# Kernel optimization log

Measured on AMD Instinct MI355X. Metric: run time of the kernel, lower is better.

The kernel has to match this reference:

```python
import jax, jax.numpy as jnp
import numpy as np

E, CAP, D = 32, 4096, 256
H = 4 * D  # hidden_dim = 4*d_model


def setup_inputs() -> dict:
    key = jax.random.key(0)
    k1, k2, k3 = jax.random.split(key, 3)
    x = jax.random.normal(k1, (E, CAP, D), dtype=jnp.float32)
    w_fc = jax.random.normal(k2, (E, D, H), dtype=jnp.float32) * (1.0 / np.sqrt(D))
    w_proj = jax.random.normal(k3, (E, H, D), dtype=jnp.float32) * (1.0 / np.sqrt(H))
    return {"x": x, "w_fc": w_fc, "w_proj": w_proj}


def reference(x, w_fc, w_proj):
    # h = bmm(x, w_fc): [E, cap, d] @ [E, d, 4d] -> [E, cap, 4d]
    h = jnp.einsum('ecd,edh->ech', x, w_fc)
    # exact GELU (torch nn.GELU default uses erf form)
    h = jax.nn.gelu(h, approximate=False)
    # out = bmm(h, w_proj): [E, cap, 4d] @ [E, 4d, d] -> [E, cap, d]
    out = jnp.einsum('ech,ehd->ecd', h, w_proj)
    # dropout is identity in eval mode (p=0.0 here)
    return out
```

## Files before the change

kernel.cpp:

```cpp
#include <hip/hip_runtime.h>
#include <cstdint>
#include <cstddef>


#define NE   32
#define CAPN 4096
#define DDIM 256
#define HDIM 1024

typedef __bf16 bf16x8 __attribute__((ext_vector_type(8)));
typedef __bf16 bf16x4 __attribute__((ext_vector_type(4)));
typedef __bf16 bf16x2 __attribute__((ext_vector_type(2)));
typedef float  f32x4  __attribute__((ext_vector_type(4)));

#define B_XS   0
#define B_HC   65536
#define B_STG  98304
#define LDS160 163840

#define AS1 __attribute__((address_space(1)))
#define AS3 __attribute__((address_space(3)))

__device__ __forceinline__ void gld_lds16(const void* g, void* l) {
  __builtin_amdgcn_global_load_lds((const AS1 uint32_t*)g, (AS3 uint32_t*)l, 16, 0, 0);
}

__device__ __forceinline__ float gelu_f(float x) {
  float x2 = x * x;
  float u  = x * __builtin_fmaf(0.1029432f, x2, 2.3022078f);
  float t  = __builtin_amdgcn_exp2f(u);
  float r  = __builtin_amdgcn_rcpf(t + 1.0f);
  return __builtin_fmaf(-x, r, x);
}

#define WAITV(n) asm volatile("s_waitcnt vmcnt(" #n ") lgkmcnt(0)" ::: "memory")
#define LGKM0()  asm volatile("s_waitcnt lgkmcnt(0)" ::: "memory")
#define BAR()    do { __builtin_amdgcn_s_barrier(); __builtin_amdgcn_sched_barrier(0); } while (0)

__global__ __launch_bounds__(256) void tcast_kernel(const float* __restrict__ in,
                                                    __bf16* __restrict__ outp,
                                                    int R, int C) {
  __shared__ __bf16 tl[64][72];
  const int cb = C >> 6;
  const int nb = (R >> 6) * cb;
  const int b  = blockIdx.x;
  const int e  = b / nb;
  const int t  = b - e * nb;
  const int br = t / cb;
  const int bc = t - br * cb;
  const float* src = in + ((size_t)e * R + (size_t)br * 64) * C + (size_t)bc * 64;
#pragma unroll
  for (int i = 0; i < 16; ++i) {
    int idx = i * 256 + threadIdx.x;
    int r = idx >> 6, c = idx & 63;
    tl[c][r] = (__bf16)src[(size_t)r * C + c];
  }
  __syncthreads();
  __bf16* dst = outp + ((size_t)e * C + (size_t)bc * 64) * R + (size_t)br * 64;
#pragma unroll
  for (int i = 0; i < 8; ++i) {
    int idx = i * 512 + threadIdx.x * 2;
    int c = idx >> 6, r = idx & 63;
    bf16x2 p;
    p[0] = tl[c][r];
    p[1] = tl[c][r + 1];
    *(bf16x2*)(dst + (size_t)c * R + r) = p;
  }
}

__global__ __launch_bounds__(512, 1) void fused_mlp(
    const float* __restrict__ x, const __bf16* __restrict__ wfcT,
    const __bf16* __restrict__ wprojT, float* __restrict__ out) {
  extern __shared__ char smem[];
  const int tid  = threadIdx.x;
  const int lane = tid & 63;
  const int l15  = lane & 15;
  const int l4   = lane >> 4;
  const int l7   = l15 & 7;
  const int w    = tid >> 6;
  const int wm   = w & 1;
  const int q    = w >> 1;
  const int e    = blockIdx.x >> 5;
  const int m0   = (blockIdx.x & 31) << 7;

  const int physA  = l4 ^ ((l15 >> 1) & 3);
  const int aOff0  = (q * 32 + l15) * 64 + physA * 16;
  const int mRow   = wm * 64 + l15;
  const int bxOff0 = mRow * 64 + physA * 16;
  const int hcOff0 = mRow * 256;
  const int pl     = l4 ^ l7;

  const float* xbase = x + ((size_t)(e * CAPN + m0)) * DDIM;
  const int xm    = tid >> 2;
  const int xsl   = tid & 3;
  const int xphys = xsl ^ ((xm >> 1) & 3);

  auto stage_slab = [&](int s) {
    const int buf = s & 3;
    const int c   = s >> 4;
    const int t   = s & 15;
    const __bf16* base;
    size_t rs;
    if (t < 8) {
      base = wfcT + ((size_t)(e * HDIM + c * 256)) * DDIM + t * 32;
      rs   = DDIM;
    } else {
      base = wprojT + ((size_t)(e * DDIM)) * HDIM + c * 256 + ((t >> 2) & 1) * 128 + (t & 3) * 32;
      rs   = HDIM;
    }
#pragma unroll
    for (int i = 0; i < 2; ++i) {
      int o  = tid + i * 512;
      int r  = o >> 2;
      int sl = (o & 3) ^ ((r >> 1) & 3);
      gld_lds16(base + (size_t)r * rs + sl * 8, &smem[B_STG + buf * 16384 + o * 16]);
    }
  };

  float4 xb0_[8], xb1_[8];

#define XLOAD(P) do {                                                          \
    const float* xs_ = xbase + (size_t)xm * DDIM + (P) * 32 + xsl * 8;         \
    xb0_[P] = *(const float4*)xs_;                                             \
    xb1_[P] = *(const float4*)(xs_ + 4);                                       \
  } while (0)

#define XCONV(P) do {                                                          \
    bf16x8 v_;                                                                 \
    v_[0] = (__bf16)xb0_[P].x; v_[1] = (__bf16)xb0_[P].y;                      \
    v_[2] = (__bf16)xb0_[P].z; v_[3] = (__bf16)xb0_[P].w;                      \
    v_[4] = (__bf16)xb1_[P].x; v_[5] = (__bf16)xb1_[P].y;                      \
    v_[6] = (__bf16)xb1_[P].z; v_[7] = (__bf16)xb1_[P].w;                      \
    *(bf16x8*)(&smem[B_XS + (P) * 8192 + xm * 64 + xphys * 16]) = v_;          \
  } while (0)

  f32x4 zero = 0.0f;
  f32x4 acc1[4][4], acc2[4][4];
#pragma unroll
  for (int a = 0; a < 4; ++a)
#pragma unroll
    for (int b = 0; b < 4; ++b) acc2[a][b] = zero;

#define ZERO_ACC1() do {                                                       \
    _Pragma("unroll") for (int a_ = 0; a_ < 4; ++a_)                           \
      _Pragma("unroll") for (int b_ = 0; b_ < 4; ++b_) acc1[a_][b_] = zero;    \
  } while (0)

#define P1SLAB(BUF, DS) do {                                                   \
    bf16x8 af_[4], bx_[4];                                                     \
    const char* sb_ = &smem[B_STG + (BUF) * 16384];                            \
    _Pragma("unroll") for (int f_ = 0; f_ < 4; ++f_)                           \
      af_[f_] = *(const bf16x8*)(sb_ + aOff0 + (f_ & 1) * 1024 + (f_ >> 1) * 8192); \
    const char* xs_ = &smem[B_XS + (DS) * 8192 + bxOff0];                      \
    _Pragma("unroll") for (int fm_ = 0; fm_ < 4; ++fm_)                        \
      bx_[fm_] = *(const bf16x8*)(xs_ + fm_ * 1024);                           \
    __builtin_amdgcn_s_setprio(1);                                             \
    _Pragma("unroll") for (int f_ = 0; f_ < 4; ++f_)                           \
      _Pragma("unroll") for (int fm_ = 0; fm_ < 4; ++fm_)                      \
        acc1[f_][fm_] = __builtin_amdgcn_mfma_f32_16x16x32_bf16(af_[f_], bx_[fm_], acc1[f_][fm_], 0, 0, 0); \
    __builtin_amdgcn_s_setprio(0);                                             \
  } while (0)

#define P2SLAB(BUF, HS) do {                                                   \
    bf16x8 af_[4], bx_[4];                                                     \
    const char* sb_ = &smem[B_STG + (BUF) * 16384];                            \
    _Pragma("unroll") for (int f_ = 0; f_ < 4; ++f_)                           \
      af_[f_] = *(const bf16x8*)(sb_ + aOff0 + (f_ & 1) * 1024 + (f_ >> 1) * 8192); \
    const int p_ = ((((HS) & 2) ? 8 : 0)) | (pl ^ (((HS) & 1) * 4));           \
    _Pragma("unroll") for (int fm_ = 0; fm_ < 4; ++fm_)                        \
      bx_[fm_] = *(const bf16x8*)(&smem[B_HC + hcOff0 + fm_ * 4096 + p_ * 16]); \
    __builtin_amdgcn_s_setprio(1);                                             \
    _Pragma("unroll") for (int f_ = 0; f_ < 4; ++f_)                           \
      _Pragma("unroll") for (int fm_ = 0; fm_ < 4; ++fm_)                      \
        acc2[f_][fm_] = __builtin_amdgcn_mfma_f32_16x16x32_bf16(af_[f_], bx_[fm_], acc2[f_][fm_], 0, 0, 0); \
    __builtin_amdgcn_s_setprio(0);                                             \
  } while (0)

#define GELU_HALF(G) do {                                                      \
    _Pragma("unroll") for (int f2_ = 0; f2_ < 2; ++f2_) {                      \
      const int s_ = q * 4 + f2_ * 2 + (l4 >> 1);                              \
      const int p_ = (s_ & 8) | ((s_ & 7) ^ l7);                               \
      _Pragma("unroll") for (int fm_ = 0; fm_ < 4; ++fm_) {                    \
        bf16x4 hv_;                                                            \
        _Pragma("unroll") for (int j_ = 0; j_ < 4; ++j_)                       \
          hv_[j_] = (__bf16)gelu_f(acc1[(G) * 2 + f2_][fm_][j_]);              \
        *(bf16x4*)(&smem[B_HC + hcOff0 + fm_ * 4096 + p_ * 16 + (l4 & 1) * 8]) = hv_; \
      }                                                                        \
    }                                                                          \
  } while (0)

#define W_C0(T, VM) do {                                                       \
    WAITV(VM); BAR();                                                          \
    stage_slab((T) + 3);                                                       \
    if ((T) <= 4) XLOAD((T) + 3);                                              \
    P1SLAB((T) & 3, (T));                                                      \
    if ((T) <= 6) XCONV((T) + 1);                                              \
  } while (0)

#define W_P1(C, T) do {                                                        \
    WAITV(4); BAR();                                                           \
    stage_slab((C) * 16 + (T) + 3);                                            \
    P1SLAB((T) & 3, (T));                                                      \
  } while (0)

#define W_P2(C, T, VM) do {                                                    \
    WAITV(VM); BAR();                                                          \
    if ((C) * 16 + (T) + 3 < 64) stage_slab((C) * 16 + (T) + 3);               \
    P2SLAB((T) & 3, ((T) - 8) & 3);                                            \
  } while (0)

#define W_P2G(C) do {   \
    WAITV(4); BAR();                                                           \
    stage_slab((C) * 16 + 15);                                                 \
    GELU_HALF(1);                                                              \
    LGKM0(); BAR();                                                            \
    P2SLAB(0, 0);                                                              \
  } while (0)

#define CHUNK_TAIL(C, VM14, VM15) do {                                         \
    GELU_HALF(0);                                                              \
    W_P2((C), 8, 4); W_P2((C), 9, 4); W_P2((C), 10, 4); W_P2((C), 11, 4);      \
    W_P2G(C);                                                                  \
    W_P2((C), 13, 4); W_P2((C), 14, VM14); W_P2((C), 15, VM15);                \
  } while (0)

  XLOAD(0); XLOAD(1); XLOAD(2);
  stage_slab(0); stage_slab(1); stage_slab(2);
  XCONV(0);

  ZERO_ACC1();
  W_C0(0, 4); W_C0(1, 6); W_C0(2, 8); W_C0(3, 10);
  W_C0(4, 10); W_C0(5, 10); W_C0(6, 8); W_C0(7, 6);
  CHUNK_TAIL(0, 4, 4);

  for (int c = 1; c < 3; ++c) {
    ZERO_ACC1();
    W_P1(c, 0); W_P1(c, 1); W_P1(c, 2); W_P1(c, 3);
    W_P1(c, 4); W_P1(c, 5); W_P1(c, 6); W_P1(c, 7);
    CHUNK_TAIL(c, 4, 4);
  }

  ZERO_ACC1();
  W_P1(3, 0); W_P1(3, 1); W_P1(3, 2); W_P1(3, 3);
  W_P1(3, 4); W_P1(3, 5); W_P1(3, 6); W_P1(3, 7);
  CHUNK_TAIL(3, 2, 0);

#pragma unroll
  for (int f = 0; f < 4; ++f) {
#pragma unroll
    for (int fm = 0; fm < 4; ++fm) {
      int m = m0 + mRow + fm * 16;
      int d = q * 32 + (f & 1) * 16 + (f >> 1) * 128 + l4 * 4;
      *(f32x4*)(out + ((size_t)(e * CAPN + m)) * DDIM + d) = acc2[f][fm];
    }
  }
}

extern "C" void kernel_launch(void* const* d_in, const int* in_sizes, int n_in,
                              void* d_out, int out_size, void* d_ws, size_t ws_size,
                              hipStream_t stream) {
  (void)in_sizes; (void)n_in; (void)out_size; (void)ws_size;
  const float* x     = (const float*)d_in[0];
  const float* wfc   = (const float*)d_in[1];
  const float* wproj = (const float*)d_in[2];
  float* out = (float*)d_out;

  __bf16* wfcT   = (__bf16*)d_ws;
  __bf16* wprojT = (__bf16*)((char*)d_ws + (size_t)NE * DDIM * HDIM * sizeof(__bf16));

  hipFuncSetAttribute((const void*)fused_mlp,
                      hipFuncAttributeMaxDynamicSharedMemorySize, LDS160);

  tcast_kernel<<<dim3(NE * 64), dim3(256), 0, stream>>>(wfc, wfcT, DDIM, HDIM);
  tcast_kernel<<<dim3(NE * 64), dim3(256), 0, stream>>>(wproj, wprojT, HDIM, DDIM);
  fused_mlp<<<dim3(NE * 32), dim3(512), LDS160, stream>>>(x, wfcT, wprojT, out);
}
```

Baseline: 221.2 us.

## Software-pipeline LDS fragment loads with double-buffered register sets across MFMA slabs

Splits each slab step into separate fragment-load and MFMA phases, using two register sets (A/B) so the LDS reads for the next slab are issued right after the current slab's MFMAs and overlap them. The staging schedule is deepened (one more slab in flight, waits changed to vmcnt(2)) and the x-conversion in the first chunk is advanced by one step. This aims to hide LDS read latency behind matrix-core work. In exchange it raises register pressure with a second fragment set and makes the barrier and buffer-reuse ordering more delicate, so reads could race with staging writes.

```diff
diff --git a/kernel.cpp b/kernel.cpp
--- a/kernel.cpp
+++ b/kernel.cpp
@@ -36,6 +36,7 @@
 #define WAITV(n) asm volatile("s_waitcnt vmcnt(" #n ") lgkmcnt(0)" ::: "memory")
 #define LGKM0()  asm volatile("s_waitcnt lgkmcnt(0)" ::: "memory")
 #define BAR()    do { __builtin_amdgcn_s_barrier(); __builtin_amdgcn_sched_barrier(0); } while (0)
+#define SB0()    __builtin_amdgcn_sched_barrier(0)
 
 __global__ __launch_bounds__(256) void tcast_kernel(const float* __restrict__ in,
                                                     __bf16* __restrict__ outp,
@@ -146,33 +147,31 @@
       _Pragma("unroll") for (int b_ = 0; b_ < 4; ++b_) acc1[a_][b_] = zero;    \
   } while (0)
 
-#define P1SLAB(BUF, DS) do {                                                   \
-    bf16x8 af_[4], bx_[4];                                                     \
-    const char* sb_ = &smem[B_STG + (BUF) * 16384];                            \
+  bf16x8 afA[4], bxA[4], afB[4], bxB[4];
+
+#define PRE_AF(SET, BUF_) do {                                                 \
+    const char* sb_ = &smem[B_STG + (BUF_) * 16384];                           \
     _Pragma("unroll") for (int f_ = 0; f_ < 4; ++f_)                           \
-      af_[f_] = *(const bf16x8*)(sb_ + aOff0 + (f_ & 1) * 1024 + (f_ >> 1) * 8192); \
-    const char* xs_ = &smem[B_XS + (DS) * 8192 + bxOff0];                      \
+      af##SET[f_] = *(const bf16x8*)(sb_ + aOff0 + (f_ & 1) * 1024 + (f_ >> 1) * 8192); \
+  } while (0)
+
+#define PRE_BX1(SET, DS_) do {                                                 \
+    const char* xs_ = &smem[B_XS + (DS_) * 8192 + bxOff0];                     \
     _Pragma("unroll") for (int fm_ = 0; fm_ < 4; ++fm_)                        \
-      bx_[fm_] = *(const bf16x8*)(xs_ + fm_ * 1024);                           \
+      bx##SET[fm_] = *(const bf16x8*)(xs_ + fm_ * 1024);                       \
+  } while (0)
+
+#define PRE_BX2(SET, HS_) do {                                                 \
+    const int p_ = (((HS_) & 2) ? 8 : 0) | (pl ^ (((HS_) & 1) * 4));           \
+    _Pragma("unroll") for (int fm_ = 0; fm_ < 4; ++fm_)                        \
+      bx##SET[fm_] = *(const bf16x8*)(&smem[B_HC + hcOff0 + fm_ * 4096 + p_ * 16]); \
+  } while (0)
+
+#define MFMA16(SET, ACC) do {                                                  \
     __builtin_amdgcn_s_setprio(1);                                             \
     _Pragma("unroll") for (int f_ = 0; f_ < 4; ++f_)                           \
       _Pragma("unroll") for (int fm_ = 0; fm_ < 4; ++fm_)                      \
-        acc1[f_][fm_] = __builtin_amdgcn_mfma_f32_16x16x32_bf16(af_[f_], bx_[fm_], acc1[f_][fm_], 0, 0, 0); \
-    __builtin_amdgcn_s_setprio(0);                                             \
-  } while (0)
-
-#define P2SLAB(BUF, HS) do {                                                   \
-    bf16x8 af_[4], bx_[4];                                                     \
-    const char* sb_ = &smem[B_STG + (BUF) * 16384];                            \
-    _Pragma("unroll") for (int f_ = 0; f_ < 4; ++f_)                           \
-      af_[f_] = *(const bf16x8*)(sb_ + aOff0 + (f_ & 1) * 1024 + (f_ >> 1) * 8192); \
-    const int p_ = ((((HS) & 2) ? 8 : 0)) | (pl ^ (((HS) & 1) * 4));           \
-    _Pragma("unroll") for (int fm_ = 0; fm_ < 4; ++fm_)                        \
-      bx_[fm_] = *(const bf16x8*)(&smem[B_HC + hcOff0 + fm_ * 4096 + p_ * 16]); \
-    __builtin_amdgcn_s_setprio(1);                                             \
-    _Pragma("unroll") for (int f_ = 0; f_ < 4; ++f_)                           \
-      _Pragma("unroll") for (int fm_ = 0; fm_ < 4; ++fm_)                      \
-        acc2[f_][fm_] = __builtin_amdgcn_mfma_f32_16x16x32_bf16(af_[f_], bx_[fm_], acc2[f_][fm_], 0, 0, 0); \
+        ACC[f_][fm_] = __builtin_amdgcn_mfma_f32_16x16x32_bf16(af##SET[f_], bx##SET[fm_], ACC[f_][fm_], 0, 0, 0); \
     __builtin_amdgcn_s_setprio(0);                                             \
   } while (0)
 
@@ -189,61 +188,73 @@
     }                                                                          \
   } while (0)
 
-#define W_C0(T, VM) do {                                                       \
-    WAITV(VM); BAR();                                                          \
-    stage_slab((T) + 3);                                                       \
-    if ((T) <= 4) XLOAD((T) + 3);                                              \
-    P1SLAB((T) & 3, (T));                                                      \
-    if ((T) <= 6) XCONV((T) + 1);                                              \
-  } while (0)
-
-#define W_P1(C, T) do {                                                        \
-    WAITV(4); BAR();                                                           \
-    stage_slab((C) * 16 + (T) + 3);                                            \
-    P1SLAB((T) & 3, (T));                                                      \
-  } while (0)
-
-#define W_P2(C, T, VM) do {                                                    \
-    WAITV(VM); BAR();                                                          \
-    if ((C) * 16 + (T) + 3 < 64) stage_slab((C) * 16 + (T) + 3);               \
-    P2SLAB((T) & 3, ((T) - 8) & 3);                                            \
-  } while (0)
-
-#define W_P2G(C) do {   \
-    WAITV(4); BAR();                                                           \
-    stage_slab((C) * 16 + 15);                                                 \
-    GELU_HALF(1);                                                              \
-    LGKM0(); BAR();                                                            \
-    P2SLAB(0, 0);                                                              \
-  } while (0)
-
-#define CHUNK_TAIL(C, VM14, VM15) do {                                         \
-    GELU_HALF(0);                                                              \
-    W_P2((C), 8, 4); W_P2((C), 9, 4); W_P2((C), 10, 4); W_P2((C), 11, 4);      \
-    W_P2G(C);                                                                  \
-    W_P2((C), 13, 4); W_P2((C), 14, VM14); W_P2((C), 15, VM15);                \
-  } while (0)
-
+#define CHUNK_HEAD(C_) do {                                                    \
+    WAITV(2); BAR(); MFMA16(A, acc1); stage_slab((C_)*16 + 3);  PRE_AF(B, 1); PRE_BX1(B, 1); \
+    WAITV(2); BAR(); MFMA16(B, acc1); stage_slab((C_)*16 + 4);  PRE_AF(A, 2); PRE_BX1(A, 2); \
+    WAITV(2); BAR(); MFMA16(A, acc1); stage_slab((C_)*16 + 5);  PRE_AF(B, 3); PRE_BX1(B, 3); \
+    WAITV(2); BAR(); MFMA16(B, acc1); stage_slab((C_)*16 + 6);  PRE_AF(A, 0); PRE_BX1(A, 4); \
+    WAITV(2); BAR(); MFMA16(A, acc1); stage_slab((C_)*16 + 7);  PRE_AF(B, 1); PRE_BX1(B, 5); \
+    WAITV(2); BAR(); MFMA16(B, acc1); stage_slab((C_)*16 + 8);  PRE_AF(A, 2); PRE_BX1(A, 6); \
+    WAITV(2); BAR(); MFMA16(A, acc1); stage_slab((C_)*16 + 9);  PRE_AF(B, 3); PRE_BX1(B, 7); \
+  } while (0)
+
+#define CHUNK_TAIL7(C_, LAST_) do {                                            \
+    WAITV(2); BAR(); MFMA16(B, acc1); GELU_HALF(0);                            \
+      stage_slab((C_)*16 + 10); PRE_AF(A, 0);                                  \
+    WAITV(2); BAR(); PRE_BX2(A, 0); MFMA16(A, acc2);                           \
+      stage_slab((C_)*16 + 11); PRE_AF(B, 1); PRE_BX2(B, 1);                   \
+    WAITV(2); BAR(); MFMA16(B, acc2); stage_slab((C_)*16 + 12);                \
+      PRE_AF(A, 2); PRE_BX2(A, 2);                                             \
+    WAITV(2); BAR(); MFMA16(A, acc2); stage_slab((C_)*16 + 13);                \
+      PRE_AF(B, 3); PRE_BX2(B, 3);                                             \
+    WAITV(2); BAR(); MFMA16(B, acc2); stage_slab((C_)*16 + 14);                \
+      PRE_AF(A, 0);                                                            \
+    WAITV(2); BAR(); GELU_HALF(1); ZERO_ACC1(); LGKM0(); BAR();                \
+      PRE_BX2(A, 0); MFMA16(A, acc2); stage_slab((C_)*16 + 15);                \
+      PRE_AF(B, 1); PRE_BX2(B, 1);                                             \
+    WAITV(2); BAR(); MFMA16(B, acc2);                                          \
+      if (!(LAST_)) stage_slab((C_)*16 + 16);                                  \
+      PRE_AF(A, 2); PRE_BX2(A, 2);                                             \
+    if (LAST_) { WAITV(0); } else { WAITV(2); }                                \
+    BAR(); MFMA16(A, acc2);                                                    \
+      if (!(LAST_)) stage_slab((C_)*16 + 17);                                  \
+      PRE_AF(B, 3); PRE_BX2(B, 3);                                             \
+    if (LAST_) { WAITV(0); } else { WAITV(2); }                                \
+    BAR(); MFMA16(B, acc2);                                                    \
+      if (!(LAST_)) { stage_slab((C_)*16 + 18); PRE_AF(A, 0); PRE_BX1(A, 0); } \
+  } while (0)
+
+  ZERO_ACC1();
   XLOAD(0); XLOAD(1); XLOAD(2);
+  SB0();
   stage_slab(0); stage_slab(1); stage_slab(2);
-  XCONV(0);
-
-  ZERO_ACC1();
-  W_C0(0, 4); W_C0(1, 6); W_C0(2, 8); W_C0(3, 10);
-  W_C0(4, 10); W_C0(5, 10); W_C0(6, 8); W_C0(7, 6);
-  CHUNK_TAIL(0, 4, 4);
+  XCONV(0); XCONV(1);
+
+  WAITV(2); BAR();
+  PRE_AF(A, 0); PRE_BX1(A, 0);
+  MFMA16(A, acc1);
+  stage_slab(3); SB0(); XLOAD(3); PRE_AF(B, 1); PRE_BX1(B, 1); XCONV(2);
+  WAITV(4); BAR(); MFMA16(B, acc1);
+  stage_slab(4); SB0(); XLOAD(4); PRE_AF(A, 2); PRE_BX1(A, 2); XCONV(3);
+  WAITV(6); BAR(); MFMA16(A, acc1);
+  stage_slab(5); SB0(); XLOAD(5); PRE_AF(B, 3); PRE_BX1(B, 3); XCONV(4);
+  WAITV(6); BAR(); MFMA16(B, acc1);
+  stage_slab(6); SB0(); XLOAD(6); PRE_AF(A, 0); PRE_BX1(A, 4); XCONV(5);
+  WAITV(6); BAR(); MFMA16(A, acc1);
+  stage_slab(7); SB0(); XLOAD(7); PRE_AF(B, 1); PRE_BX1(B, 5); XCONV(6);
+  WAITV(6); BAR(); MFMA16(B, acc1);
+  stage_slab(8); PRE_AF(A, 2); PRE_BX1(A, 6); XCONV(7);
+  WAITV(4); BAR(); MFMA16(A, acc1);
+  stage_slab(9); PRE_AF(B, 3); PRE_BX1(B, 7);
+  CHUNK_TAIL7(0, 0);
 
   for (int c = 1; c < 3; ++c) {
-    ZERO_ACC1();
-    W_P1(c, 0); W_P1(c, 1); W_P1(c, 2); W_P1(c, 3);
-    W_P1(c, 4); W_P1(c, 5); W_P1(c, 6); W_P1(c, 7);
-    CHUNK_TAIL(c, 4, 4);
-  }
-
-  ZERO_ACC1();
-  W_P1(3, 0); W_P1(3, 1); W_P1(3, 2); W_P1(3, 3);
-  W_P1(3, 4); W_P1(3, 5); W_P1(3, 6); W_P1(3, 7);
-  CHUNK_TAIL(3, 2, 0);
+    CHUNK_HEAD(c);
+    CHUNK_TAIL7(c, 0);
+  }
+
+  CHUNK_HEAD(3);
+  CHUNK_TAIL7(3, 1);
 
 #pragma unroll
   for (int f = 0; f < 4; ++f) {
```

After: 216.5 us. 1.02x faster.

## Software-pipeline LDS fragment reads with double-buffered registers across MFMA steps

Applied to the files above, without the earlier changes.

Restructures the fused MoE MLP main loop so the LDS fragment loads for the next slab go into a second register set while the current slab's MFMAs run. The stage-slab lambda is replaced by precomputed per-thread global offsets in specialized FC and projection staging macros. Most waits drop the lgkmcnt(0) requirement, leaving only vmcnt waits. This is meant to hide LDS latency and cut address arithmetic, at the cost of more VGPRs for the double fragment registers and tighter correctness dependencies between buffer reuse and barriers.

```diff
diff --git a/kernel.cpp b/kernel.cpp
--- a/kernel.cpp
+++ b/kernel.cpp
@@ -33,9 +33,12 @@
   return __builtin_fmaf(-x, r, x);
 }
 
-#define WAITV(n) asm volatile("s_waitcnt vmcnt(" #n ") lgkmcnt(0)" ::: "memory")
-#define LGKM0()  asm volatile("s_waitcnt lgkmcnt(0)" ::: "memory")
-#define BAR()    do { __builtin_amdgcn_s_barrier(); __builtin_amdgcn_sched_barrier(0); } while (0)
+#define WV_(n)  asm volatile("s_waitcnt vmcnt(" #n ")" ::: "memory")
+#define WV(n)   WV_(n)
+#define WVL_(n) asm volatile("s_waitcnt vmcnt(" #n ") lgkmcnt(0)" ::: "memory")
+#define WVL(n)  WVL_(n)
+#define LGKM0() asm volatile("s_waitcnt lgkmcnt(0)" ::: "memory")
+#define BAR()   do { __builtin_amdgcn_s_barrier(); __builtin_amdgcn_sched_barrier(0); } while (0)
 
 __global__ __launch_bounds__(256) void tcast_kernel(const float* __restrict__ in,
                                                     __bf16* __restrict__ outp,
@@ -90,32 +93,31 @@
   const int hcOff0 = mRow * 256;
   const int pl     = l4 ^ l7;
 
+  const int rr  = tid >> 2;
+  const int ssl = (tid & 3) ^ ((rr >> 1) & 3);
+  const int gofsFC = rr * DDIM + ssl * 8;
+  const int gofsPJ = rr * HDIM + ssl * 8;
+  const __bf16* wfcT_e   = wfcT   + (size_t)e * HDIM * DDIM;
+  const __bf16* wprojT_e = wprojT + (size_t)e * DDIM * HDIM;
+  char* ldsStg0 = smem + B_STG + tid * 16;
+
   const float* xbase = x + ((size_t)(e * CAPN + m0)) * DDIM;
   const int xm    = tid >> 2;
   const int xsl   = tid & 3;
   const int xphys = xsl ^ ((xm >> 1) & 3);
 
-  auto stage_slab = [&](int s) {
-    const int buf = s & 3;
-    const int c   = s >> 4;
-    const int t   = s & 15;
-    const __bf16* base;
-    size_t rs;
-    if (t < 8) {
-      base = wfcT + ((size_t)(e * HDIM + c * 256)) * DDIM + t * 32;
-      rs   = DDIM;
-    } else {
-      base = wprojT + ((size_t)(e * DDIM)) * HDIM + c * 256 + ((t >> 2) & 1) * 128 + (t & 3) * 32;
-      rs   = HDIM;
-    }
-#pragma unroll
-    for (int i = 0; i < 2; ++i) {
-      int o  = tid + i * 512;
-      int r  = o >> 2;
-      int sl = (o & 3) ^ ((r >> 1) & 3);
-      gld_lds16(base + (size_t)r * rs + sl * 8, &smem[B_STG + buf * 16384 + o * 16]);
-    }
-  };
+#define STAGE_FC(C_, T_) do {                                                  \
+    const __bf16* s0_ = wfcT_e + (size_t)(C_) * (256 * DDIM) + (T_) * 32 + gofsFC; \
+    gld_lds16(s0_,              ldsStg0 + ((T_) & 3) * 16384);                 \
+    gld_lds16(s0_ + 128 * DDIM, ldsStg0 + ((T_) & 3) * 16384 + 8192);          \
+  } while (0)
+
+#define STAGE_PJ(C_, T_) do {                                                  \
+    const __bf16* s0_ = wprojT_e + (size_t)(C_) * 256 +                        \
+                        (((T_) >> 2) & 1) * 128 + ((T_) & 3) * 32 + gofsPJ;    \
+    gld_lds16(s0_,              ldsStg0 + ((T_) & 3) * 16384);                 \
+    gld_lds16(s0_ + 128 * HDIM, ldsStg0 + ((T_) & 3) * 16384 + 8192);          \
+  } while (0)
 
   float4 xb0_[8], xb1_[8];
 
@@ -139,40 +141,38 @@
 #pragma unroll
   for (int a = 0; a < 4; ++a)
 #pragma unroll
-    for (int b = 0; b < 4; ++b) acc2[a][b] = zero;
+    for (int b = 0; b < 4; ++b) { acc1[a][b] = zero; acc2[a][b] = zero; }
 
 #define ZERO_ACC1() do {                                                       \
     _Pragma("unroll") for (int a_ = 0; a_ < 4; ++a_)                           \
       _Pragma("unroll") for (int b_ = 0; b_ < 4; ++b_) acc1[a_][b_] = zero;    \
   } while (0)
 
-#define P1SLAB(BUF, DS) do {                                                   \
-    bf16x8 af_[4], bx_[4];                                                     \
-    const char* sb_ = &smem[B_STG + (BUF) * 16384];                            \
+  bf16x8 afR0[4], bxR0[4], afR1[4], bxR1[4];
+
+#define PAF(S_, BUF_) do {                                                     \
+    const char* sb_ = smem + B_STG + (BUF_) * 16384;                           \
     _Pragma("unroll") for (int f_ = 0; f_ < 4; ++f_)                           \
-      af_[f_] = *(const bf16x8*)(sb_ + aOff0 + (f_ & 1) * 1024 + (f_ >> 1) * 8192); \
-    const char* xs_ = &smem[B_XS + (DS) * 8192 + bxOff0];                      \
+      afR##S_[f_] = *(const bf16x8*)(sb_ + aOff0 + (f_ & 1) * 1024 + (f_ >> 1) * 8192); \
+  } while (0)
+
+#define PBX1(S_, DS_) do {                                                     \
+    const char* xs_ = smem + B_XS + (DS_) * 8192 + bxOff0;                     \
     _Pragma("unroll") for (int fm_ = 0; fm_ < 4; ++fm_)                        \
-      bx_[fm_] = *(const bf16x8*)(xs_ + fm_ * 1024);                           \
+      bxR##S_[fm_] = *(const bf16x8*)(xs_ + fm_ * 1024);                       \
+  } while (0)
+
+#define PBX2(S_, HS_) do {                                                     \
+    const int p_ = ((((HS_) & 2) ? 8 : 0)) | (pl ^ (((HS_) & 1) * 4));         \
+    _Pragma("unroll") for (int fm_ = 0; fm_ < 4; ++fm_)                        \
+      bxR##S_[fm_] = *(const bf16x8*)(&smem[B_HC + hcOff0 + fm_ * 4096 + p_ * 16]); \
+  } while (0)
+
+#define MFMA16(S_, ACC_) do {                                                  \
     __builtin_amdgcn_s_setprio(1);                                             \
     _Pragma("unroll") for (int f_ = 0; f_ < 4; ++f_)                           \
       _Pragma("unroll") for (int fm_ = 0; fm_ < 4; ++fm_)                      \
-        acc1[f_][fm_] = __builtin_amdgcn_mfma_f32_16x16x32_bf16(af_[f_], bx_[fm_], acc1[f_][fm_], 0, 0, 0); \
-    __builtin_amdgcn_s_setprio(0);                                             \
-  } while (0)
-
-#define P2SLAB(BUF, HS) do {                                                   \
-    bf16x8 af_[4], bx_[4];                                                     \
-    const char* sb_ = &smem[B_STG + (BUF) * 16384];                            \
-    _Pragma("unroll") for (int f_ = 0; f_ < 4; ++f_)                           \
-      af_[f_] = *(const bf16x8*)(sb_ + aOff0 + (f_ & 1) * 1024 + (f_ >> 1) * 8192); \
-    const int p_ = ((((HS) & 2) ? 8 : 0)) | (pl ^ (((HS) & 1) * 4));           \
-    _Pragma("unroll") for (int fm_ = 0; fm_ < 4; ++fm_)                        \
-      bx_[fm_] = *(const bf16x8*)(&smem[B_HC + hcOff0 + fm_ * 4096 + p_ * 16]); \
-    __builtin_amdgcn_s_setprio(1);                                             \
-    _Pragma("unroll") for (int f_ = 0; f_ < 4; ++f_)                           \
-      _Pragma("unroll") for (int fm_ = 0; fm_ < 4; ++fm_)                      \
-        acc2[f_][fm_] = __builtin_amdgcn_mfma_f32_16x16x32_bf16(af_[f_], bx_[fm_], acc2[f_][fm_], 0, 0, 0); \
+        ACC_[f_][fm_] = __builtin_amdgcn_mfma_f32_16x16x32_bf16(afR##S_[f_], bxR##S_[fm_], ACC_[f_][fm_], 0, 0, 0); \
     __builtin_amdgcn_s_setprio(0);                                             \
   } while (0)
 
@@ -189,61 +189,102 @@
     }                                                                          \
   } while (0)
 
-#define W_C0(T, VM) do {                                                       \
-    WAITV(VM); BAR();                                                          \
-    stage_slab((T) + 3);                                                       \
-    if ((T) <= 4) XLOAD((T) + 3);                                              \
-    P1SLAB((T) & 3, (T));                                                      \
-    if ((T) <= 6) XCONV((T) + 1);                                              \
-  } while (0)
-
-#define W_P1(C, T) do {                                                        \
-    WAITV(4); BAR();                                                           \
-    stage_slab((C) * 16 + (T) + 3);                                            \
-    P1SLAB((T) & 3, (T));                                                      \
-  } while (0)
-
-#define W_P2(C, T, VM) do {                                                    \
-    WAITV(VM); BAR();                                                          \
-    if ((C) * 16 + (T) + 3 < 64) stage_slab((C) * 16 + (T) + 3);               \
-    P2SLAB((T) & 3, ((T) - 8) & 3);                                            \
-  } while (0)
-
-#define W_P2G(C) do {   \
-    WAITV(4); BAR();                                                           \
-    stage_slab((C) * 16 + 15);                                                 \
-    GELU_HALF(1);                                                              \
-    LGKM0(); BAR();                                                            \
-    P2SLAB(0, 0);                                                              \
-  } while (0)
-
-#define CHUNK_TAIL(C, VM14, VM15) do {                                         \
-    GELU_HALF(0);                                                              \
-    W_P2((C), 8, 4); W_P2((C), 9, 4); W_P2((C), 10, 4); W_P2((C), 11, 4);      \
-    W_P2G(C);                                                                  \
-    W_P2((C), 13, 4); W_P2((C), 14, VM14); W_P2((C), 15, VM15);                \
-  } while (0)
-
   XLOAD(0); XLOAD(1); XLOAD(2);
-  stage_slab(0); stage_slab(1); stage_slab(2);
-  XCONV(0);
-
-  ZERO_ACC1();
-  W_C0(0, 4); W_C0(1, 6); W_C0(2, 8); W_C0(3, 10);
-  W_C0(4, 10); W_C0(5, 10); W_C0(6, 8); W_C0(7, 6);
-  CHUNK_TAIL(0, 4, 4);
+  STAGE_FC(0, 0); STAGE_FC(0, 1); STAGE_FC(0, 2);
+  XCONV(0); XCONV(1);
+
+  WVL(2); BAR();
+  PAF(0, 0); PBX1(0, 0);
+  MFMA16(0, acc1);
+  XLOAD(3); STAGE_FC(0, 3); PAF(1, 1); PBX1(1, 1); XCONV(2);
+  WVL(2); BAR(); MFMA16(1, acc1);
+  XLOAD(4); STAGE_FC(0, 4); PAF(0, 2); PBX1(0, 2); XCONV(3);
+  WVL(2); BAR(); MFMA16(0, acc1);
+  XLOAD(5); STAGE_FC(0, 5); PAF(1, 3); PBX1(1, 3); XCONV(4);
+  WVL(2); BAR(); MFMA16(1, acc1);
+  XLOAD(6); STAGE_FC(0, 6); PAF(0, 0); PBX1(0, 4); XCONV(5);
+  WVL(2); BAR(); MFMA16(0, acc1);
+  XLOAD(7); STAGE_FC(0, 7); PAF(1, 1); PBX1(1, 5); XCONV(6);
+  WVL(2); BAR(); MFMA16(1, acc1);
+  STAGE_PJ(0, 8); PAF(0, 2); PBX1(0, 6); XCONV(7);
+  WVL(2); BAR(); MFMA16(0, acc1);
+  STAGE_PJ(0, 9); PAF(1, 3); PBX1(1, 7);
+  WVL(2); BAR(); MFMA16(1, acc1);
+  STAGE_PJ(0, 10); PAF(0, 0); GELU_HALF(0);
+
+#define CHUNK_TAIL(C_) do {                                                    \
+    WVL(2); BAR(); PBX2(0, 0); MFMA16(0, acc2);                       \
+    STAGE_PJ(C_, 11); PAF(1, 1); PBX2(1, 1);                                   \
+    WV(2); BAR(); MFMA16(1, acc2);                                    \
+    STAGE_PJ(C_, 12); PAF(0, 2); PBX2(0, 2);                                   \
+    WV(2); BAR(); MFMA16(0, acc2);                                    \
+    STAGE_PJ(C_, 13); PAF(1, 3); PBX2(1, 3);                                   \
+    WV(2); BAR(); MFMA16(1, acc2);                                    \
+    STAGE_PJ(C_, 14); PAF(0, 0);                                               \
+    WV(2); BAR(); GELU_HALF(1); ZERO_ACC1(); LGKM0(); BAR();          \
+    PBX2(0, 0); MFMA16(0, acc2);                                               \
+    STAGE_PJ(C_, 15); PAF(1, 1); PBX2(1, 1);                                   \
+  } while (0)
+
+  CHUNK_TAIL(0);
+  WV(2); BAR(); MFMA16(1, acc2);
+  STAGE_FC(1, 0); PAF(0, 2); PBX2(0, 2);
+  WV(2); BAR(); MFMA16(0, acc2);
+  STAGE_FC(1, 1); PAF(1, 3); PBX2(1, 3);
+  WV(2); BAR(); MFMA16(1, acc2);
+  STAGE_FC(1, 2); PAF(0, 0); PBX1(0, 0);
 
   for (int c = 1; c < 3; ++c) {
-    ZERO_ACC1();
-    W_P1(c, 0); W_P1(c, 1); W_P1(c, 2); W_P1(c, 3);
-    W_P1(c, 4); W_P1(c, 5); W_P1(c, 6); W_P1(c, 7);
-    CHUNK_TAIL(c, 4, 4);
-  }
-
-  ZERO_ACC1();
-  W_P1(3, 0); W_P1(3, 1); W_P1(3, 2); W_P1(3, 3);
-  W_P1(3, 4); W_P1(3, 5); W_P1(3, 6); W_P1(3, 7);
-  CHUNK_TAIL(3, 2, 0);
+    WV(2); BAR(); MFMA16(0, acc1);
+    STAGE_FC(c, 3); PAF(1, 1); PBX1(1, 1);
+    WV(2); BAR(); MFMA16(1, acc1);
+    STAGE_FC(c, 4); PAF(0, 2); PBX1(0, 2);
+    WV(2); BAR(); MFMA16(0, acc1);
+    STAGE_FC(c, 5); PAF(1, 3); PBX1(1, 3);
+    WV(2); BAR(); MFMA16(1, acc1);
+    STAGE_FC(c, 6); PAF(0, 0); PBX1(0, 4);
+    WV(2); BAR(); MFMA16(0, acc1);
+    STAGE_FC(c, 7); PAF(1, 1); PBX1(1, 5);
+    WV(2); BAR(); MFMA16(1, acc1);
+    STAGE_PJ(c, 8); PAF(0, 2); PBX1(0, 6);
+    WV(2); BAR(); MFMA16(0, acc1);
+    STAGE_PJ(c, 9); PAF(1, 3); PBX1(1, 7);
+    WV(2); BAR(); MFMA16(1, acc1);
+    STAGE_PJ(c, 10); PAF(0, 0); GELU_HALF(0);
+    CHUNK_TAIL(c);
+    WV(2); BAR(); MFMA16(1, acc2);
+    STAGE_FC(c + 1, 0); PAF(0, 2); PBX2(0, 2);
+    WV(2); BAR(); MFMA16(0, acc2);
+    STAGE_FC(c + 1, 1); PAF(1, 3); PBX2(1, 3);
+    WV(2); BAR(); MFMA16(1, acc2);
+    STAGE_FC(c + 1, 2); PAF(0, 0); PBX1(0, 0);
+  }
+
+  {
+    const int c = 3;
+    WV(2); BAR(); MFMA16(0, acc1);
+    STAGE_FC(c, 3); PAF(1, 1); PBX1(1, 1);
+    WV(2); BAR(); MFMA16(1, acc1);
+    STAGE_FC(c, 4); PAF(0, 2); PBX1(0, 2);
+    WV(2); BAR(); MFMA16(0, acc1);
+    STAGE_FC(c, 5); PAF(1, 3); PBX1(1, 3);
+    WV(2); BAR(); MFMA16(1, acc1);
+    STAGE_FC(c, 6); PAF(0, 0); PBX1(0, 4);
+    WV(2); BAR(); MFMA16(0, acc1);
+    STAGE_FC(c, 7); PAF(1, 1); PBX1(1, 5);
+    WV(2); BAR(); MFMA16(1, acc1);
+    STAGE_PJ(c, 8); PAF(0, 2); PBX1(0, 6);
+    WV(2); BAR(); MFMA16(0, acc1);
+    STAGE_PJ(c, 9); PAF(1, 3); PBX1(1, 7);
+    WV(2); BAR(); MFMA16(1, acc1);
+    STAGE_PJ(c, 10); PAF(0, 0); GELU_HALF(0);
+    CHUNK_TAIL(c);
+    WV(2); BAR(); MFMA16(1, acc2);
+    PAF(0, 2); PBX2(0, 2);
+    WV(0); BAR(); MFMA16(0, acc2);
+    PAF(1, 3); PBX2(1, 3);
+    WV(0); BAR(); MFMA16(1, acc2);
+  }
 
 #pragma unroll
   for (int f = 0; f < 4; ++f) {
```

Result: faster. 210.1 us (-5.0%).
